# Kernel optimization log

Hardware: AMD Instinct MI355X
Metric: run time of the kernel (lower is better)

Reference implementation:

```python
import jax, jax.numpy as jnp
import numpy as np

B, T, I, H, L = 256, 2000, 80, 20, 2
G = 4 * H  # gates i,f,g,o (PyTorch order)


def _lstm_dir(xg, w_hh, reverse):
    # xg: [B, T, 4H] precomputed input-gate contributions (incl. bias)
    # w_hh: [H, 4H]
    xg_t = jnp.swapaxes(xg, 0, 1)  # [T, B, 4H]
    if reverse:
        xg_t = xg_t[::-1]

    def step(carry, g_x):
        h, c = carry
        gates = g_x + h @ w_hh  # [B, 4H]
        i, f, g, o = jnp.split(gates, 4, axis=-1)
        c = jax.nn.sigmoid(f) * c + jax.nn.sigmoid(i) * jnp.tanh(g)
        h = jax.nn.sigmoid(o) * jnp.tanh(c)
        return (h, c), h

    h0 = jnp.zeros((xg.shape[0], H), xg.dtype)
    _, hs = jax.lax.scan(step, (h0, h0), xg_t)  # hs: [T, B, H]
    if reverse:
        hs = hs[::-1]
    return jnp.swapaxes(hs, 0, 1)  # [B, T, H]


def _bilstm_layer(x, w_ih, w_hh, b):
    # x: [B, T, in], w_ih: [2, in, 4H], w_hh: [2, H, 4H], b: [2, 4H]
    out = []
    for d in range(2):
        xg = jnp.einsum('bti,ig->btg', x, w_ih[d]) + b[d]
        out.append(_lstm_dir(xg, w_hh[d], reverse=(d == 1)))
    return jnp.concatenate(out, axis=-1)  # [B, T, 2H]


def setup_inputs() -> dict:
    key = jax.random.key(0)
    ks = jax.random.split(key, 9)
    s = 1.0 / np.sqrt(H)
    u = lambda k, shp: jax.random.uniform(k, shp, jnp.float32, -s, s)
    return {
        'x': jax.random.normal(ks[0], (B, T, I), jnp.float32),
        'w_ih_l0': u(ks[1], (2, I, G)),
        'w_hh_l0': u(ks[2], (2, H, G)),
        'b_l0': u(ks[3], (2, G)),
        'w_ih_l1': u(ks[4], (2, 2 * H, G)),
        'w_hh_l1': u(ks[5], (2, H, G)),
        'b_l1': u(ks[6], (2, G)),
        'fc_w': u(ks[7], (1, 2 * H)),
        'fc_b': u(ks[8], (1,)),
    }


def reference(x, w_ih_l0, w_hh_l0, b_l0, w_ih_l1, w_hh_l1, b_l1, fc_w, fc_b):
    h = _bilstm_layer(x, w_ih_l0, w_hh_l0, b_l0)      # [B, T, 2H]
    h = _bilstm_layer(h, w_ih_l1, w_hh_l1, b_l1)      # [B, T, 2H]
    out = h @ fc_w.T + fc_b                           # [B, T, 1]
    return out.squeeze(-1)                            # [B, T]
```

## Files before the change

### kernel.cpp

```cpp
#include <hip/hip_runtime.h>
#include <math.h>

#define B_ 256
#define T_ 2000
#define I_ 80
#define H_ 20
#define G_ 80
#define M_ 512000

#define LOG2E 1.442695041f

typedef __attribute__((ext_vector_type(2))) float f32x2;
typedef __attribute__((ext_vector_type(2))) unsigned u32x2;

__device__ __forceinline__ f32x2 mk2(float a, float b) { f32x2 r; r.x = a; r.y = b; return r; }

__device__ __forceinline__ float swap_half(float x, int swapidx) {
#if __has_builtin(__builtin_amdgcn_permlane32_swap)
    u32x2 r = __builtin_amdgcn_permlane32_swap(__float_as_uint(x), __float_as_uint(x), false, false);
    return __uint_as_float(r.y);
#else
    return __uint_as_float((unsigned)__builtin_amdgcn_ds_bpermute(swapidx, (int)__float_as_uint(x)));
#endif
}

#define WS2_STRIDE 332
#define WS2_SIZE   6640

template<int K>
__global__ __launch_bounds__(256) void gemm_xg(
    const float* __restrict__ X,
    const float* __restrict__ Wih,
    const float* __restrict__ Bias,
    float* __restrict__ XG,
    int M)
{
    constexpr int KC = 40;
    __shared__ float ws2[WS2_SIZE];
    __shared__ float xs[KC][100];
    __shared__ float bs[160];

    const int tid  = threadIdx.x;
    const int row0 = blockIdx.x * 96;
    const int tx = tid % 20;
    const int ty = tid / 20;
    const bool run = (ty < 12);

    if (tid < 160) {
        int dd = (tid >= 80);
        int r = tid - 80 * dd;
        int j = r >> 2, g = r & 3;
        float sc = (g == 2) ? 2.0f * LOG2E : -LOG2E;
        bs[tid] = sc * Bias[dd * 80 + g * 20 + j];
    }

    int nrows = M - row0; if (nrows > 96) nrows = 96;

    f32x2 acc[8][4];
    bool first = true;
    const float* wsp = &ws2[tx * WS2_STRIDE];

    for (int kc = 0; kc < K; kc += KC) {
        for (int idx = tid; idx < KC * 160; idx += 256) {
            int i = idx / 160, cc = idx - 160 * i;
            int dd = (cc >= 80), r = cc - 80 * dd;
            int j = r >> 2, g = r & 3;
            float sc = (g == 2) ? 2.0f * LOG2E : -LOG2E;
            ws2[(cc >> 3) * WS2_STRIDE + i * 8 + (cc & 7)] =
                sc * Wih[(dd * K + kc + i) * 80 + g * 20 + j];
        }
        for (int i4 = tid; i4 < (96 * KC) / 4; i4 += 256) {
            int r = i4 / 10;
            int kk = (i4 - 10 * r) * 4;
            float4 v = make_float4(0.f, 0.f, 0.f, 0.f);
            if (r < nrows)
                v = *(const float4*)(X + (long long)(row0 + r) * K + kc + kk);
            xs[kk][r] = v.x; xs[kk + 1][r] = v.y; xs[kk + 2][r] = v.z; xs[kk + 3][r] = v.w;
        }
        __syncthreads();

        if (first) {
            first = false;
            #pragma unroll
            for (int p = 0; p < 4; ++p) {
                const f32x2 bv = mk2(bs[tx * 8 + 2 * p], bs[tx * 8 + 2 * p + 1]);
                #pragma unroll
                for (int r = 0; r < 8; ++r) acc[r][p] = bv;
            }
        }

        if (run) {
            #pragma unroll 4
            for (int k = 0; k < KC; ++k) {
                float a[8];
                f32x2 b2[4];
                *(float4*)&a[0]  = *(const float4*)&xs[k][ty * 8];
                *(float4*)&a[4]  = *(const float4*)&xs[k][ty * 8 + 4];
                *(float4*)&b2[0] = *(const float4*)&wsp[k * 8];
                *(float4*)&b2[2] = *(const float4*)&wsp[k * 8 + 4];
                #pragma unroll
                for (int r = 0; r < 8; ++r) {
                    const f32x2 av = mk2(a[r], a[r]);
                    #pragma unroll
                    for (int p = 0; p < 4; ++p)
                        acc[r][p] = __builtin_elementwise_fma(av, b2[p], acc[r][p]);
                }
            }
        }
        __syncthreads();
    }

    if (run) {
        #pragma unroll
        for (int r = 0; r < 8; ++r) {
            int row = row0 + ty * 8 + r;
            if (row < M) {
                float* dst = XG + (long long)row * 160 + tx * 8;
                *(float4*)(dst)     = *(float4*)&acc[r][0];
                *(float4*)(dst + 4) = *(float4*)&acc[r][2];
            }
        }
    }
}

__device__ __forceinline__ void scan_dir(
    const float* __restrict__ xg,
    const float* __restrict__ w_hh,
    float* __restrict__ h_out,
    int T, int b, int d, int lane)
{
    const int half = lane >> 5;
    const int j    = lane & 31;
    const bool act_lane = (lane < H_);
    const int jj   = (j < H_) ? j : 0;
    const bool isB = (d == 1);

    const int swapidx = ((lane + 32) & 63) << 2;

    const int gA = half ? 2 : 0;
    const int gB = gA + 1;
    const float scA = half ? (2.0f * LOG2E) : (-LOG2E);
    const float scB = -LOG2E;

    f32x2 wA[10], wB[10];
    const float* wb = w_hh + d * (H_ * G_);
    #pragma unroll
    for (int i = 0; i < 10; ++i) {
        wA[i] = mk2(scA * wb[(2 * i) * G_ + gA * 20 + jj],
                    scA * wb[(2 * i + 1) * G_ + gA * 20 + jj]);
        wB[i] = mk2(scB * wb[(2 * i) * G_ + gB * 20 + jj],
                    scB * wb[(2 * i + 1) * G_ + gB * 20 + jj]);
    }

    float sh[20];
    #pragma unroll
    for (int k = 0; k < 20; ++k) sh[k] = 0.f;
    float c = 0.f;

    const int t0    = isB ? (T - 1) : 0;
    const int rstep = isB ? -160 : 160;
    const float* pf = xg + ((long long)(b * T + t0) * 2 + d) * 80 + 4 * jj + 2 * half;

    float* hp = h_out + ((long long)b * 40 + d * 20 + jj) * T + (isB ? T - 4 : 0);
    const int hgstep = isB ? -4 : 4;

    constexpr int PF = 8;
    f32x2 px[PF];
    #pragma unroll
    for (int s = 0; s < PF; ++s) { px[s] = *(const f32x2*)pf; pf += rstep; }

    float hq0 = 0.f, hq1 = 0.f, hq2 = 0.f, hq3 = 0.f;

    for (int tb = 0; tb < T; tb += PF) {
        #pragma unroll
        for (int s = 0; s < PF; ++s) {
            const f32x2 v = px[s];
            px[s] = *(const f32x2*)pf; pf += rstep;

            f32x2 aA1 = mk2(v.x, 0.f);
            f32x2 aA2 = mk2(0.f, 0.f);
            f32x2 aB1 = mk2(v.y, 0.f);
            f32x2 aB2 = mk2(0.f, 0.f);
            #pragma unroll
            for (int i = 0; i < 5; ++i) {
                const f32x2 hlo = mk2(sh[2 * i],      sh[2 * i + 1]);
                const f32x2 hhi = mk2(sh[10 + 2 * i], sh[11 + 2 * i]);
                aA1 = __builtin_elementwise_fma(wA[i],     hlo, aA1);
                aA2 = __builtin_elementwise_fma(wA[i + 5], hhi, aA2);
                aB1 = __builtin_elementwise_fma(wB[i],     hlo, aB1);
                aB2 = __builtin_elementwise_fma(wB[i + 5], hhi, aB2);
            }
            const f32x2 tA = aA1 + aA2;
            const f32x2 tB = aB1 + aB2;
            const float mA = tA.x + tA.y;
            const float mB = tB.x + tB.y;

            const float sA = __builtin_amdgcn_rcpf(1.0f + __builtin_amdgcn_exp2f(mA));
            const float sB = __builtin_amdgcn_rcpf(1.0f + __builtin_amdgcn_exp2f(mB));

            const float sAx = swap_half(sA, swapidx);
            const float gox = swap_half(sB, swapidx);

            const float gg = fmaf(-2.0f, sAx, 1.0f);
            c = fmaf(sB, c, sA * gg);
            const float th = fmaf(-2.0f,
                __builtin_amdgcn_rcpf(1.0f + __builtin_amdgcn_exp2f(2.0f * LOG2E * c)), 1.0f);
            const float hj = gox * th;

            {
                const int p = s & 3;
                if (p == 0) hq0 = hj;
                else if (p == 1) hq1 = hj;
                else if (p == 2) hq2 = hj;
                else {
                    hq3 = hj;
                    float4 sv;
                    sv.x = isB ? hq3 : hq0;
                    sv.y = isB ? hq2 : hq1;
                    sv.z = isB ? hq1 : hq2;
                    sv.w = isB ? hq0 : hq3;
                    if (act_lane) *(float4*)hp = sv;
                    hp += hgstep;
                }
            }

            #pragma unroll
            for (int k = 0; k < 20; ++k)
                sh[k] = __uint_as_float(__builtin_amdgcn_readlane(__float_as_uint(hj), k));
        }
    }
}

__global__ __launch_bounds__(512) void scan0_gemm1(
    float* __restrict__ xg,
    const float* __restrict__ whh0,
    const float* __restrict__ wih1,
    const float* __restrict__ b1,
    float* __restrict__ h0t,
    int T)
{
    __shared__ float ws2s[WS2_SIZE];
    __shared__ float xs[40][100];
    __shared__ float bs[160];

    const int b   = blockIdx.x;
    const int tid = threadIdx.x;

    if (tid >= 128) {
        for (int idx = tid - 128; idx < 40 * 160; idx += 384) {
            int i = idx / 160, cc = idx - 160 * i;
            int dd = (cc >= 80), r = cc - 80 * dd;
            int jc = r >> 2, g = r & 3;
            float sc = (g == 2) ? 2.0f * LOG2E : -LOG2E;
            ws2s[(cc >> 3) * WS2_STRIDE + i * 8 + (cc & 7)] =
                sc * wih1[(dd * 40 + i) * 80 + g * 20 + jc];
        }
        if (tid - 128 < 160) {
            int cidx = tid - 128;
            int dd = (cidx >= 80);
            int r = cidx - 80 * dd;
            int jc = r >> 2, g = r & 3;
            float sc = (g == 2) ? 2.0f * LOG2E : -LOG2E;
            bs[cidx] = sc * b1[dd * 80 + g * 20 + jc];
        }
    } else {
        scan_dir(xg, whh0, h0t, T, b, tid >> 6, tid & 63);
    }
    __syncthreads();

    const int tx  = tid % 20;
    const int tyy = tid / 20;
    const bool run = (tyy < 24);
    const float* wsp = &ws2s[tx * WS2_STRIDE];

    for (int tc = 0; tc < 21; ++tc) {
        const int t0 = tc * 96;
        int nrows = T - t0; if (nrows > 96) nrows = 96;

        for (int i4 = tid; i4 < 40 * 24; i4 += 512) {
            int k = i4 / 24;
            int r = (i4 - 24 * k) * 4;
            float4 v = make_float4(0.f, 0.f, 0.f, 0.f);
            if (r < nrows)
                v = *(const float4*)(h0t + ((long long)b * 40 + k) * T + t0 + r);
            *(float4*)&xs[k][r] = v;
        }
        __syncthreads();

        if (run) {
            f32x2 acc[4][4];
            #pragma unroll
            for (int p = 0; p < 4; ++p) {
                const f32x2 bv = mk2(bs[tx * 8 + 2 * p], bs[tx * 8 + 2 * p + 1]);
                #pragma unroll
                for (int r = 0; r < 4; ++r) acc[r][p] = bv;
            }
            #pragma unroll 4
            for (int k = 0; k < 40; ++k) {
                float a[4];
                f32x2 b2[4];
                *(float4*)&a[0]  = *(const float4*)&xs[k][tyy * 4];
                *(float4*)&b2[0] = *(const float4*)&wsp[k * 8];
                *(float4*)&b2[2] = *(const float4*)&wsp[k * 8 + 4];
                #pragma unroll
                for (int r = 0; r < 4; ++r) {
                    const f32x2 av = mk2(a[r], a[r]);
                    #pragma unroll
                    for (int p = 0; p < 4; ++p)
                        acc[r][p] = __builtin_elementwise_fma(av, b2[p], acc[r][p]);
                }
            }
            #pragma unroll
            for (int r = 0; r < 4; ++r) {
                int rr = tyy * 4 + r;
                if (rr < nrows) {
                    long long row = (long long)b * T + t0 + rr;
                    float* dst = xg + row * 160 + tx * 8;
                    *(float4*)(dst)     = *(float4*)&acc[r][0];
                    *(float4*)(dst + 4) = *(float4*)&acc[r][2];
                }
            }
        }
        __syncthreads();
    }
}

__global__ __launch_bounds__(512) void scan1_fc(
    const float* __restrict__ xg,
    const float* __restrict__ whh1,
    const float* __restrict__ fcw,
    const float* __restrict__ fcb,
    float* __restrict__ h1t,
    float* __restrict__ out,
    int T)
{
    const int b   = blockIdx.x;
    const int tid = threadIdx.x;

    if (tid < 128)
        scan_dir(xg, whh1, h1t, T, b, tid >> 6, tid & 63);
    __syncthreads();

    const int t = tid * 4;
    if (t <= T - 4) {
        const float bias = fcb[0];
        float4 acc = make_float4(bias, bias, bias, bias);
        const float* base = h1t + (long long)b * 40 * T + t;
        #pragma unroll 8
        for (int u = 0; u < 40; ++u) {
            const float wv = fcw[u];
            const float4 hv = *(const float4*)(base + (long long)u * T);
            acc.x = fmaf(hv.x, wv, acc.x);
            acc.y = fmaf(hv.y, wv, acc.y);
            acc.z = fmaf(hv.z, wv, acc.z);
            acc.w = fmaf(hv.w, wv, acc.w);
        }
        *(float4*)(out + (long long)b * T + t) = acc;
    }
}

extern "C" void kernel_launch(void* const* d_in, const int* in_sizes, int n_in,
                              void* d_out, int out_size, void* d_ws, size_t ws_size,
                              hipStream_t stream) {
    const float* x     = (const float*)d_in[0];
    const float* wih0  = (const float*)d_in[1];
    const float* whh0  = (const float*)d_in[2];
    const float* b0    = (const float*)d_in[3];
    const float* wih1  = (const float*)d_in[4];
    const float* whh1  = (const float*)d_in[5];
    const float* b1    = (const float*)d_in[6];
    const float* fcw   = (const float*)d_in[7];
    const float* fcb   = (const float*)d_in[8];
    float* out = (float*)d_out;

    float* ws  = (float*)d_ws;
    float* xg  = ws + 2048;
    float* h0t = xg + 81920000LL + 2048;
    float* h1t = h0t + 20480000LL;

    const int M = M_;
    const int gemm_grid = (M + 95) / 96;

    gemm_xg<80><<<dim3(gemm_grid), dim3(256), 0, stream>>>(x, wih0, b0, xg, M);
    scan0_gemm1<<<dim3(B_), dim3(512), 0, stream>>>(xg, whh0, wih1, b1, h0t, T_);
    scan1_fc<<<dim3(B_), dim3(512), 0, stream>>>(xg, whh1, fcw, fcb, h1t, out, T_);
}
```

Before: 1.371 ms.

## Make layer-0 input GEMM persistent with full weight cached in LDS

After: 1.347 ms. Within noise of the previous version (-1.8%).

```diff
diff --git a/kernel.cpp b/kernel.cpp
--- a/kernel.cpp
+++ b/kernel.cpp
@@ -26,26 +26,34 @@
 
 #define WS2_STRIDE 332
 #define WS2_SIZE   6640
-
-template<int K>
-__global__ __launch_bounds__(256) void gemm_xg(
+#define WSF_STRIDE 644
+#define WSF_SIZE   12880
+
+__global__ __launch_bounds__(256) void gemm_xg_p(
     const float* __restrict__ X,
     const float* __restrict__ Wih,
     const float* __restrict__ Bias,
     float* __restrict__ XG,
-    int M)
+    int M, int ntiles, int nblocks)
 {
-    constexpr int KC = 40;
-    __shared__ float ws2[WS2_SIZE];
-    __shared__ float xs[KC][100];
+    constexpr int K = 80;
+    __shared__ float wsf[WSF_SIZE];
+    __shared__ float xs[40][100];
     __shared__ float bs[160];
 
-    const int tid  = threadIdx.x;
-    const int row0 = blockIdx.x * 96;
-    const int tx = tid % 20;
-    const int ty = tid / 20;
+    const int tid = threadIdx.x;
+    const int tx  = tid % 20;
+    const int ty  = tid / 20;
     const bool run = (ty < 12);
 
+    for (int idx = tid; idx < K * 160; idx += 256) {
+        int i = idx / 160, cc = idx - 160 * i;
+        int dd = (cc >= 80), r = cc - 80 * dd;
+        int j = r >> 2, g = r & 3;
+        float sc = (g == 2) ? 2.0f * LOG2E : -LOG2E;
+        wsf[(cc >> 3) * WSF_STRIDE + i * 8 + (cc & 7)] =
+            sc * Wih[(dd * K + i) * 80 + g * 20 + j];
+    }
     if (tid < 160) {
         int dd = (tid >= 80);
         int r = tid - 80 * dd;
@@ -53,71 +61,67 @@
         float sc = (g == 2) ? 2.0f * LOG2E : -LOG2E;
         bs[tid] = sc * Bias[dd * 80 + g * 20 + j];
     }
-
-    int nrows = M - row0; if (nrows > 96) nrows = 96;
-
-    f32x2 acc[8][4];
-    bool first = true;
-    const float* wsp = &ws2[tx * WS2_STRIDE];
-
-    for (int kc = 0; kc < K; kc += KC) {
-        for (int idx = tid; idx < KC * 160; idx += 256) {
-            int i = idx / 160, cc = idx - 160 * i;
-            int dd = (cc >= 80), r = cc - 80 * dd;
-            int j = r >> 2, g = r & 3;
-            float sc = (g == 2) ? 2.0f * LOG2E : -LOG2E;
-            ws2[(cc >> 3) * WS2_STRIDE + i * 8 + (cc & 7)] =
-                sc * Wih[(dd * K + kc + i) * 80 + g * 20 + j];
-        }
-        for (int i4 = tid; i4 < (96 * KC) / 4; i4 += 256) {
-            int r = i4 / 10;
-            int kk = (i4 - 10 * r) * 4;
-            float4 v = make_float4(0.f, 0.f, 0.f, 0.f);
-            if (r < nrows)
-                v = *(const float4*)(X + (long long)(row0 + r) * K + kc + kk);
-            xs[kk][r] = v.x; xs[kk + 1][r] = v.y; xs[kk + 2][r] = v.z; xs[kk + 3][r] = v.w;
-        }
-        __syncthreads();
-
-        if (first) {
-            first = false;
-            #pragma unroll
-            for (int p = 0; p < 4; ++p) {
-                const f32x2 bv = mk2(bs[tx * 8 + 2 * p], bs[tx * 8 + 2 * p + 1]);
-                #pragma unroll
-                for (int r = 0; r < 8; ++r) acc[r][p] = bv;
-            }
-        }
-
-        if (run) {
-            #pragma unroll 4
-            for (int k = 0; k < KC; ++k) {
-                float a[8];
-                f32x2 b2[4];
-                *(float4*)&a[0]  = *(const float4*)&xs[k][ty * 8];
-                *(float4*)&a[4]  = *(const float4*)&xs[k][ty * 8 + 4];
-                *(float4*)&b2[0] = *(const float4*)&wsp[k * 8];
-                *(float4*)&b2[2] = *(const float4*)&wsp[k * 8 + 4];
-                #pragma unroll
-                for (int r = 0; r < 8; ++r) {
-                    const f32x2 av = mk2(a[r], a[r]);
-                    #pragma unroll
-                    for (int p = 0; p < 4; ++p)
-                        acc[r][p] = __builtin_elementwise_fma(av, b2[p], acc[r][p]);
-                }
-            }
-        }
-        __syncthreads();
-    }
-
-    if (run) {
+    __syncthreads();
+
+    const float* wsp = &wsf[tx * WSF_STRIDE];
+    const f32x2 bv0 = mk2(bs[tx * 8 + 0], bs[tx * 8 + 1]);
+    const f32x2 bv1 = mk2(bs[tx * 8 + 2], bs[tx * 8 + 3]);
+    const f32x2 bv2 = mk2(bs[tx * 8 + 4], bs[tx * 8 + 5]);
+    const f32x2 bv3 = mk2(bs[tx * 8 + 6], bs[tx * 8 + 7]);
+
+    for (int tile = blockIdx.x; tile < ntiles; tile += nblocks) {
+        const int row0 = tile * 96;
+        int nrows = M - row0; if (nrows > 96) nrows = 96;
+
+        f32x2 acc[8][4];
         #pragma unroll
         for (int r = 0; r < 8; ++r) {
-            int row = row0 + ty * 8 + r;
-            if (row < M) {
-                float* dst = XG + (long long)row * 160 + tx * 8;
-                *(float4*)(dst)     = *(float4*)&acc[r][0];
-                *(float4*)(dst + 4) = *(float4*)&acc[r][2];
+            acc[r][0] = bv0; acc[r][1] = bv1; acc[r][2] = bv2; acc[r][3] = bv3;
+        }
+
+        #pragma unroll
+        for (int kc = 0; kc < K; kc += 40) {
+            for (int i4 = tid; i4 < (96 * 40) / 4; i4 += 256) {
+                int r = i4 / 10;
+                int kk = (i4 - 10 * r) * 4;
+                float4 v = make_float4(0.f, 0.f, 0.f, 0.f);
+                if (r < nrows)
+                    v = *(const float4*)(X + (long long)(row0 + r) * K + kc + kk);
+                xs[kk][r] = v.x; xs[kk + 1][r] = v.y; xs[kk + 2][r] = v.z; xs[kk + 3][r] = v.w;
+            }
+            __syncthreads();
+
+            if (run) {
+                const float* wck = wsp + kc * 8;
+                #pragma unroll 4
+                for (int k = 0; k < 40; ++k) {
+                    float a[8];
+                    f32x2 b2[4];
+                    *(float4*)&a[0]  = *(const float4*)&xs[k][ty * 8];
+                    *(float4*)&a[4]  = *(const float4*)&xs[k][ty * 8 + 4];
+                    *(float4*)&b2[0] = *(const float4*)&wck[k * 8];
+                    *(float4*)&b2[2] = *(const float4*)&wck[k * 8 + 4];
+                    #pragma unroll
+                    for (int r = 0; r < 8; ++r) {
+                        const f32x2 av = mk2(a[r], a[r]);
+                        #pragma unroll
+                        for (int p = 0; p < 4; ++p)
+                            acc[r][p] = __builtin_elementwise_fma(av, b2[p], acc[r][p]);
+                    }
+                }
+            }
+            __syncthreads();
+        }
+
+        if (run) {
+            #pragma unroll
+            for (int r = 0; r < 8; ++r) {
+                int row = row0 + ty * 8 + r;
+                if (row < M) {
+                    float* dst = XG + (long long)row * 160 + tx * 8;
+                    *(float4*)(dst)     = *(float4*)&acc[r][0];
+                    *(float4*)(dst + 4) = *(float4*)&acc[r][2];
+                }
             }
         }
     }
@@ -231,6 +235,7 @@
     }
 }
 
+__attribute__((amdgpu_waves_per_eu(2, 2)))
 __global__ __launch_bounds__(512) void scan0_gemm1(
     float* __restrict__ xg,
     const float* __restrict__ whh0,
@@ -325,6 +330,7 @@
     }
 }
 
+__attribute__((amdgpu_waves_per_eu(2, 2)))
 __global__ __launch_bounds__(512) void scan1_fc(
     const float* __restrict__ xg,
     const float* __restrict__ whh1,
@@ -379,9 +385,10 @@
     float* h1t = h0t + 20480000LL;
 
     const int M = M_;
-    const int gemm_grid = (M + 95) / 96;
-
-    gemm_xg<80><<<dim3(gemm_grid), dim3(256), 0, stream>>>(x, wih0, b0, xg, M);
+    const int ntiles = (M + 95) / 96;
+    const int nblocks = 2048;
+
+    gemm_xg_p<<<dim3(nblocks), dim3(256), 0, stream>>>(x, wih0, b0, xg, M, ntiles, nblocks);
     scan0_gemm1<<<dim3(B_), dim3(512), 0, stream>>>(xg, whh0, wih1, b1, h0t, T_);
     scan1_fc<<<dim3(B_), dim3(512), 0, stream>>>(xg, whh1, fcw, fcb, h1t, out, T_);
 }
```
